# Kernel optimization log

Hardware: AMD Instinct MI355X
Metric: run time of the kernel (lower is better)

Reference implementation:

```python
import jax, jax.numpy as jnp
import numpy as np

EPS_OT = 0.05   # sinkhorn epsilon
ITERS = 3       # sinkhorn iterations
NH = 8          # attention heads


def _l2norm(x, axis):
    return x / jnp.maximum(jnp.linalg.norm(x, axis=axis, keepdims=True), 1e-12)


def _conv(x, w, pad):
    return jax.lax.conv_general_dilated(
        x, w, (1, 1), ((pad, pad), (pad, pad)),
        dimension_numbers=("NCHW", "OIHW", "NCHW"))


def _head(x, w1, b1, g, beta, w2, b2):
    # Conv3x3 -> BatchNorm (train-mode batch stats) -> ReLU -> Conv1x1
    h = _conv(x, w1, 1) + b1[None, :, None, None]
    mu = jnp.mean(h, (0, 2, 3), keepdims=True)
    var = jnp.var(h, (0, 2, 3), keepdims=True)
    h = jax.nn.relu((h - mu) / jnp.sqrt(var + 1e-5) * g[None, :, None, None]
                    + beta[None, :, None, None])
    return jnp.einsum("oc,bchw->bohw", w2, h) + b2[None, :, None, None]


def setup_inputs() -> dict:
    key = jax.random.key(0)
    ks = jax.random.split(key, 20)
    B, C, H, W, TD = 8, 256, 48, 48, 512
    s = 0.02
    f32 = jnp.float32
    d = {
        "img_feat": jax.random.normal(ks[0], (B, C, H, W), f32),
        "txt_feat": jax.random.normal(ks[1], (B, TD), f32),
        "density_map": jax.random.uniform(ks[2], (B, 1, H, W), f32),
        "tp_w": s * jax.random.normal(ks[3], (C, TD), f32), "tp_b": jnp.zeros((C,), f32),
        "wq": s * jax.random.normal(ks[4], (C, C), f32), "bq": jnp.zeros((C,), f32),
        "wk": s * jax.random.normal(ks[5], (C, C), f32), "bk": jnp.zeros((C,), f32),
        "wv": s * jax.random.normal(ks[6], (C, C), f32), "bv": jnp.zeros((C,), f32),
        "wo": s * jax.random.normal(ks[7], (C, C), f32), "bo": jnp.zeros((C,), f32),
        "ln_g": jnp.ones((C,), f32), "ln_b": jnp.zeros((C,), f32),
        "op_w": s * jax.random.normal(ks[8], (C, C), f32), "op_b": jnp.zeros((C,), f32),
        "h1_w": s * jax.random.normal(ks[9], (C // 2, C, 3, 3), f32), "h1_b": jnp.zeros((C // 2,), f32),
        "h_bn_g": jnp.ones((C // 2,), f32), "h_bn_b": jnp.zeros((C // 2,), f32),
        "h2_w": s * jax.random.normal(ks[10], (2, C // 2), f32), "h2_b": jnp.zeros((2,), f32),
        "v1_w": s * jax.random.normal(ks[11], (C // 2, C, 3, 3), f32), "v1_b": jnp.zeros((C // 2,), f32),
        "v_bn_g": jnp.ones((C // 2,), f32), "v_bn_b": jnp.zeros((C // 2,), f32),
        "v2_w": s * jax.random.normal(ks[12], (2, C // 2), f32), "v2_b": jnp.zeros((2,), f32),
        "temperature": 0.07 * jnp.ones((1,), f32),
        "spatial_weight": 0.1 * jnp.ones((1,), f32),
    }
    return d


def reference(img_feat, txt_feat, density_map, tp_w, tp_b, wq, bq, wk, bk,
              wv, bv, wo, bo, ln_g, ln_b, op_w, op_b, h1_w, h1_b, h_bn_g,
              h_bn_b, h2_w, h2_b, v1_w, v1_b, v_bn_g, v_bn_b, v2_w, v2_b,
              temperature, spatial_weight):
    B, C, H, W = img_feat.shape
    N = H * W
    hd = C // NH

    # ---- text projection (single text token) ----
    txt_emb = txt_feat @ tp_w.T + tp_b                      # [B,C]

    # ---- cross attention: query = pixels, key/value = 1 text token ----
    img_flat = img_feat.reshape(B, C, N).transpose(0, 2, 1)  # [B,N,C]
    q = (img_flat @ wq.T + bq).reshape(B, N, NH, hd)
    k = (txt_emb @ wk.T + bk).reshape(B, 1, NH, hd)
    v = (txt_emb @ wv.T + bv).reshape(B, 1, NH, hd)
    scores = jnp.einsum("bnhd,bkhd->bhnk", q, k) / jnp.sqrt(jnp.float32(hd))
    attn = jax.nn.softmax(scores, axis=-1)                  # ones (k len = 1)
    ctx = jnp.einsum("bhnk,bkhd->bnhd", attn, v).reshape(B, N, C)
    attn_out = ctx @ wo.T + bo

    # ---- residual + layernorm ----
    x = img_flat + attn_out
    mu = jnp.mean(x, -1, keepdims=True)
    var = jnp.var(x, -1, keepdims=True)
    source_feat = (x - mu) / jnp.sqrt(var + 1e-5) * ln_g + ln_b   # [B,N,C]
    mod_img_feat = source_feat.transpose(0, 2, 1).reshape(B, C, H, W)

    # ---- target distribution q from density map ----
    target = jax.nn.relu(density_map.reshape(B, N)) + 1e-6
    q_dist = target / jnp.sum(target, axis=1, keepdims=True)

    # ---- source distribution p from cosine similarity ----
    img_n = _l2norm(mod_img_feat, 1)                        # [B,C,H,W]
    txt_n = _l2norm(txt_emb, 1)                             # [B,C]
    cos = jnp.sum(img_n * txt_n[:, :, None, None], axis=1).reshape(B, N)
    temp = jnp.clip(temperature, 0.01, None)                # [1]
    logits = cos / temp
    mask = (cos > 0.0).astype(jnp.float32)
    shifted = logits - jnp.max(logits, axis=1, keepdims=True)
    p_un = jnp.exp(shifted) * mask + 1e-8
    p = p_un / jnp.sum(p_un, axis=1, keepdims=True)

    # ---- cost matrix: feature + spatial ----
    src_n = _l2norm(source_feat, 2)                         # [B,N,C]
    feature_cost = 1.0 - jnp.einsum("bnc,bmc->bnm", src_n, src_n)
    gy, gx = jnp.meshgrid(jnp.linspace(0.0, 1.0, H), jnp.linspace(0.0, 1.0, W),
                          indexing="ij")
    coords = jnp.stack([gy, gx], -1).reshape(N, 2)
    d2 = jnp.sum((coords[:, None, :] - coords[None, :, :]) ** 2, -1)
    spatial_cost = jnp.sqrt(jnp.maximum(d2, 0.0)) / 1.41421356  # [N,N]
    cost = feature_cost + spatial_weight * spatial_cost[None]   # [B,N,N]

    # ---- log-domain Sinkhorn ----
    log_p = jnp.log(p + 1e-12)
    log_q = jnp.log(q_dist + 1e-12)
    f = jnp.zeros_like(p)
    g = jnp.zeros_like(q_dist)
    for _ in range(ITERS):
        f = EPS_OT * (log_p - jax.scipy.special.logsumexp(
            (g[:, None, :] - cost) / EPS_OT, axis=2))
        g = EPS_OT * (log_q - jax.scipy.special.logsumexp(
            (f[:, :, None] - cost) / EPS_OT, axis=1))
    T = jnp.exp((f[:, :, None] + g[:, None, :] - cost) / EPS_OT)

    # ---- transport features: T^T @ source ----
    fused = jnp.einsum("bnm,bnc->bmc", T, source_feat)      # [B,N,C]
    fused_feat = fused.transpose(0, 2, 1).reshape(B, C, H, W)

    out_feat = img_feat + (jnp.einsum("oc,bchw->bohw", op_w, fused_feat)
                           + op_b[None, :, None, None])
    heatmap_logits = _head(out_feat, h1_w, h1_b, h_bn_g, h_bn_b, h2_w, h2_b)
    hv_logits = _head(out_feat, v1_w, v1_b, v_bn_g, v_bn_b, v2_w, v2_b)
    return out_feat, heatmap_logits, hv_logits
```

## Files before the change

kernel.cpp:

```cpp
#include <hip/hip_runtime.h>
#include <hip/hip_bf16.h>

#define NTOK 2304
#define CCH  256
#define BB   8

typedef __attribute__((ext_vector_type(4))) float f32x4;
typedef __attribute__((ext_vector_type(8))) short s16x8;
typedef __attribute__((ext_vector_type(8))) _Float16 h16x8;
typedef unsigned short u16;
typedef unsigned char u8;

__device__ __forceinline__ u16 f2bf(float x){
  union{float f; unsigned u;} v; v.f = x;
  unsigned r = v.u + 0x7fffu + ((v.u>>16)&1u);
  return (u16)(r>>16);
}
__device__ __forceinline__ float bf2f(u16 h){
  union{float f; unsigned u;} v; v.u = ((unsigned)h)<<16; return v.f;
}

#if __has_builtin(__builtin_amdgcn_cvt_f32_fp8) && __has_builtin(__builtin_amdgcn_cvt_pk_fp8_f32)
#define HWFP8 1
#else
#define HWFP8 0
#endif

__device__ __forceinline__ u8 enc8(float z){
  union{float f; unsigned u;} a; a.f = fabsf(z) * 0x1p-120f;
  unsigned u = a.u + 0x7FFFFu + ((a.u>>20)&1u);
  unsigned b = (u>>20)&0x7Fu;
  if (b > 0x7Eu) b = 0x7Eu;
  return (u8)(b | (z<0.f ? 0x80u : 0u));
}
__device__ __forceinline__ float dec8(unsigned b){
  union{unsigned u; float f;} w;
  w.u = ((b&0x80u)<<24) | ((b&0x7Fu)<<20);
  return w.f * 0x1p120f;
}

#if HWFP8
__device__ __forceinline__ float DEC8(unsigned w, int e){
  switch(e & 3){
    case 0:  return __builtin_amdgcn_cvt_f32_fp8((int)w, 0);
    case 1:  return __builtin_amdgcn_cvt_f32_fp8((int)w, 1);
    case 2:  return __builtin_amdgcn_cvt_f32_fp8((int)w, 2);
    default: return __builtin_amdgcn_cvt_f32_fp8((int)w, 3);
  }
}
__device__ __forceinline__ unsigned pack4(float z0,float z1,float z2,float z3){
  int v = __builtin_amdgcn_cvt_pk_fp8_f32(z0, z1, 0, false);
  v = __builtin_amdgcn_cvt_pk_fp8_f32(z2, z3, v, true);
  return (unsigned)v;
}
#else
__device__ __forceinline__ float DEC8(unsigned w, int e){
  return dec8((w>>(8*(e&3)))&0xFFu);
}
__device__ __forceinline__ unsigned pack4(float z0,float z1,float z2,float z3){
  return (unsigned)enc8(z0) | ((unsigned)enc8(z1)<<8) |
         ((unsigned)enc8(z2)<<16) | ((unsigned)enc8(z3)<<24);
}
#endif

__device__ __forceinline__ int swz512(int row, int b){ return row*512 + (b ^ ((row&7)<<4)); }
__device__ __forceinline__ int swz128(int row, int b){ return row*128 + (b ^ ((row&7)<<4)); }
__device__ __forceinline__ int swz64 (int row, int b){ return row*64  + (b ^ ((row&3)<<4)); }

__device__ __forceinline__ void gl_lds16(const void* g, void* l){
  __builtin_amdgcn_global_load_lds(
      (const __attribute__((address_space(1))) unsigned int*)g,
      (__attribute__((address_space(3))) unsigned int*)l, 16, 0, 0);
}

struct CanonArgs {
  const void* src[31];
  int n[31];
  int off[31];
};

__global__ void k_detect(const u16* probe, int* flag){
  if (threadIdx.x==0){
    int cnt=0;
    for (int i=0;i<16;++i){
      unsigned e = (probe[2*i]>>7)&0xFFu;
      if (e>=100u && e<=140u) ++cnt;
    }
    *flag = (cnt>=14)?1:0;
  }
}

__global__ __launch_bounds__(256) void k_canon(CanonArgs a, float* dst, const int* flag, int nt){
  int t = blockIdx.y;
  if (t>=nt) return;
  int n = a.n[t];
  const void* s = a.src[t];
  float* d = dst + a.off[t];
  bool isbf = (*flag)!=0;
  int n4 = n >> 2;
  for (int i = blockIdx.x*256+threadIdx.x; i < n4; i += gridDim.x*256){
    if (isbf){
      ushort4 v = ((const ushort4*)s)[i];
      float4 o; o.x=bf2f(v.x); o.y=bf2f(v.y); o.z=bf2f(v.z); o.w=bf2f(v.w);
      ((float4*)d)[i] = o;
    } else {
      ((float4*)d)[i] = ((const float4*)s)[i];
    }
  }
  int base = n4<<2;
  int rem = n - base;
  int i = blockIdx.x*256+threadIdx.x;
  if (i < rem)
    d[base+i] = isbf ? bf2f(((const u16*)s)[base+i]) : ((const float*)s)[base+i];
}

__global__ __launch_bounds__(256) void k_txt(const float* txt, const float* tpw, const float* tpb,
    const float* wv, const float* bv, const float* wo, const float* bo, float* TXTN, float* AVEC){
  int b=blockIdx.x, t=threadIdx.x;
  __shared__ float sT[512];
  __shared__ float sE[256];
  __shared__ float sV[256];
  __shared__ float red[4];
  sT[t]      = txt[b*512+t];
  sT[t+256]  = txt[b*512+256+t];
  __syncthreads();
  float acc = tpb[t];
  const float* wr = tpw + (size_t)t*512;
  for (int k=0;k<512;++k) acc = fmaf(sT[k], wr[k], acc);
  sE[t] = acc;
  float ss = acc*acc;
  for (int d=1; d<64; d<<=1) ss += __shfl_xor(ss, d);
  if ((t&63)==0) red[t>>6] = ss;
  __syncthreads();
  float nrm = sqrtf(red[0]+red[1]+red[2]+red[3]);
  TXTN[b*256+t] = acc / fmaxf(nrm, 1e-12f);
  float av = bv[t];
  const float* wvr = wv + (size_t)t*256;
  for (int k=0;k<256;++k) av = fmaf(sE[k], wvr[k], av);
  sV[t] = av;
  __syncthreads();
  float ao = bo[t];
  const float* wor = wo + (size_t)t*256;
  for (int k=0;k<256;++k) ao = fmaf(sV[k], wor[k], ao);
  AVEC[b*256+t] = ao;
}

__global__ __launch_bounds__(256) void k_lnfuse(const float* img, const float* AVEC, const float* lng,
    const float* lnb, const float* TXTN, u16* SF, u16* SN, float* COS){
  int b=blockIdx.y, n0=blockIdx.x*32, t=threadIdx.x;
  __shared__ float xt[32][256];
  float av = AVEC[b*256+t];
  const float* ip = img + ((size_t)b*256 + t)*NTOK + n0;
  #pragma unroll
  for (int j4=0;j4<8;++j4){
    float4 v = *(const float4*)(ip + j4*4);
    xt[j4*4+0][t]=v.x+av; xt[j4*4+1][t]=v.y+av; xt[j4*4+2][t]=v.z+av; xt[j4*4+3][t]=v.w+av;
  }
  int wv_=t>>6, l=t&63;
  float lg[4], lb[4], tn[4];
  #pragma unroll
  for (int k=0;k<4;++k){ lg[k]=lng[l+64*k]; lb[k]=lnb[l+64*k]; tn[k]=TXTN[b*256+l+64*k]; }
  __syncthreads();
  for (int rr=0; rr<8; ++rr){
    int j = wv_*8+rr; int n = n0+j;
    float x[4]; float s=0.f, ss=0.f;
    #pragma unroll
    for (int k=0;k<4;++k){ float v=xt[j][l+64*k]; x[k]=v; s+=v; ss=fmaf(v,v,ss); }
    for (int d=1; d<64; d<<=1){ s += __shfl_xor(s,d); ss += __shfl_xor(ss,d); }
    float mu = s*(1.f/256.f);
    float var = ss*(1.f/256.f) - mu*mu;
    float rstd = rsqrtf(fmaxf(var,0.f)+1e-5f);
    float y[4]; float sy=0.f;
    #pragma unroll
    for (int k=0;k<4;++k){ y[k] = fmaf((x[k]-mu)*rstd, lg[k], lb[k]); sy = fmaf(y[k],y[k],sy); }
    for (int d=1; d<64; d<<=1) sy += __shfl_xor(sy,d);
    float rn = 1.f/fmaxf(sqrtf(sy),1e-12f);
    float cp = 0.f;
    size_t base = ((size_t)b*NTOK + n)*CCH;
    #pragma unroll
    for (int k=0;k<4;++k){
      float sv = y[k]*rn;
      SF[base + l+64*k] = f2bf(y[k]);
      SN[base + l+64*k] = f2bf(sv);
      cp = fmaf(sv, tn[k], cp);
    }
    for (int d=1; d<64; d<<=1) cp += __shfl_xor(cp,d);
    if (l==0) COS[b*NTOK+n] = cp;
  }
}

__global__ __launch_bounds__(256) void k_pqred(const float* COS, const float* den, const float* tmpp, float* PQS){
  int b=blockIdx.x, t=threadIdx.x;
  __shared__ float red[256];
  float temp = fmaxf(tmpp[0], 0.01f);
  float mx = -1e30f;
  for (int n=t; n<NTOK; n+=256) mx = fmaxf(mx, COS[b*NTOK+n]);
  red[t]=mx; __syncthreads();
  for (int o=128;o>0;o>>=1){ if (t<o) red[t]=fmaxf(red[t],red[t+o]); __syncthreads(); }
  float maxc = red[0]; __syncthreads();
  float sp=0.f, st=0.f;
  for (int n=t; n<NTOK; n+=256){
    float cv = COS[b*NTOK+n];
    sp += __expf((cv-maxc)/temp)*((cv>0.f)?1.f:0.f)+1e-8f;
    float dv = den[b*NTOK+n];
    st += fmaxf(dv,0.f)+1e-6f;
  }
  red[t]=sp; __syncthreads();
  for (int o=128;o>0;o>>=1){ if (t<o) red[t]+=red[t+o]; __syncthreads(); }
  sp = red[0]; __syncthreads();
  red[t]=st; __syncthreads();
  for (int o=128;o>0;o>>=1){ if (t<o) red[t]+=red[t+o]; __syncthreads(); }
  if (t==0){ PQS[b*4]=maxc; PQS[b*4+1]=sp; PQS[b*4+2]=red[0]; }
}

__global__ __launch_bounds__(256) void k_pqelem(const float* COS, const float* den, const float* tmpp,
    const float* PQS, float* LOGP, float* LOGQ, float* GV, float* CY, float* CX){
  int idx = blockIdx.x*256+threadIdx.x;
  float temp = fmaxf(tmpp[0], 0.01f);
  if (idx < BB*NTOK){
    int b = idx / NTOK;
    float maxc = PQS[b*4], sp = PQS[b*4+1], st = PQS[b*4+2];
    float cv = COS[idx];
    float pu = __expf((cv-maxc)/temp)*((cv>0.f)?1.f:0.f)+1e-8f;
    LOGP[idx] = logf(pu/sp + 1e-12f);
    float dv = den[idx];
    LOGQ[idx] = logf((fmaxf(dv,0.f)+1e-6f)/st + 1e-12f);
    GV[idx] = 0.f;
  }
  if (idx < NTOK){
    int h = idx/48, w = idx - h*48;
    CY[idx] = (float)h*(1.f/47.f);
    CX[idx] = (float)w*(1.f/47.f);
  }
}

__global__ __launch_bounds__(256) void k_packw(const float* h1w, const float* v1w, u16* W1P){
  int idx = blockIdx.x*256+threadIdx.x;
  int head = idx / 294912;
  int rem = idx - head*294912;
  int oc = rem / 2304;
  int k = rem - oc*2304;
  int tap = k >> 8;
  int c = k & 255;
  const float* src = head ? v1w : h1w;
  W1P[idx] = f2bf(src[(oc*256 + c)*9 + tap]);
}

__global__ __launch_bounds__(256) void k_trans(const u16* SF, u16* SFT){
  int n0 = blockIdx.x*64, c0 = blockIdx.y*64, b = blockIdx.z;
  __shared__ u16 tl[64][68];
  int t = threadIdx.x;
  int nl = t>>3, c8 = (t&7)*8;
  #pragma unroll
  for (int p=0;p<2;++p){
    int n = nl + p*32;
    s16x8 v = *(const s16x8*)(SF + ((size_t)(b*NTOK + n0+n)*CCH + c0 + c8));
    #pragma unroll
    for (int e=0;e<8;++e) tl[c8+e][n] = (u16)v[e];
  }
  __syncthreads();
  int cl = t>>3, n8 = (t&7)*8;
  #pragma unroll
  for (int p=0;p<2;++p){
    int c = cl + p*32;
    union{ s16x8 v; u16 us[8]; } pk;
    #pragma unroll
    for (int e=0;e<8;++e){ int s = n8+e; pk.us[e] = tl[c][((s&3)<<4) | (s>>2)]; }
    *(s16x8*)(SFT + ((size_t)(b*CCH + c0+c)*NTOK + n0 + n8)) = pk.v;
  }
}

__global__ __launch_bounds__(256, 4) void k_cost(const u16* SN, const float* CY, const float* CX,
    const float* swp, u8* Z, float* PZ, int b_base){
  int zb = blockIdx.z, b = b_base + zb;
  int i0 = blockIdx.x*64, by = blockIdx.y, j0b = by*256;
  const u16* SNb = SN + (size_t)b*NTOK*CCH;
  u8* Zb = Z + (size_t)zb*NTOK*NTOK;
  __shared__ __align__(16) char Bs[64*512];
  int tid=threadIdx.x, w=tid>>6, l=tid&63, g4=l>>4, lc=l&15;
  float spw = swp[0]*(20.0f/1.41421356f);
  const u16* Arow = SNb + (size_t)(i0 + w*16 + lc)*CCH + g4*8;
  s16x8 af[8];
  #pragma unroll
  for (int ks=0; ks<8; ++ks) af[ks] = *(const s16x8*)(Arow + ks*32);
  int mrow = w*16 + g4*4;
  float cyi[4], cxi[4];
  #pragma unroll
  for (int r=0;r<4;++r){ int i = i0+mrow+r; cyi[r]=CY[i]; cxi[r]=CX[i]; }
  float Srow[4] = {0.f,0.f,0.f,0.f};
  for (int js=0; js<4; ++js){
    int j0 = j0b + js*64;
    __syncthreads();
    #pragma unroll
    for (int u=0; u<8; ++u){
      int row = u*8 + w*2 + (l>>5);
      int src = ((l&31)*16) ^ ((row&7)<<4);
      gl_lds16((const char*)(SNb + (size_t)(j0+row)*CCH) + src, Bs + u*4096 + w*1024);
    }
    __syncthreads();
    f32x4 acc[4];
    #pragma unroll
    for (int cf=0;cf<4;++cf) acc[cf] = (f32x4){0.f,0.f,0.f,0.f};
    #pragma unroll
    for (int ks=0; ks<8; ++ks){
      int kb = ks*64 + g4*16;
      #pragma unroll
      for (int cf=0; cf<4; ++cf){
        s16x8 bb = *(const s16x8*)(Bs + swz512(cf*16+lc, kb));
        acc[cf] = __builtin_amdgcn_mfma_f32_16x16x32_bf16(af[ks], bb, acc[cf], 0,0,0);
      }
    }
    float zf[4][4];
    #pragma unroll
    for (int cf=0; cf<4; ++cf){
      int j = j0 + cf*16 + lc;
      float cyj = CY[j], cxj = CX[j];
      #pragma unroll
      for (int r=0;r<4;++r){
        float dy = cyi[r]-cyj, dx = cxi[r]-cxj;
        zf[cf][r] = (acc[cf][r]-1.0f)*20.0f - spw*sqrtf(fmaf(dy,dy,dx*dx));
      }
    }
    size_t zrow = (size_t)(i0+mrow)*NTOK + j0 + lc*4;
    #pragma unroll
    for (int r=0;r<4;++r){
      unsigned pw = pack4(zf[0][r], zf[1][r], zf[2][r], zf[3][r]);
      Srow[r] += __expf(DEC8(pw,0)) + __expf(DEC8(pw,1))
               + __expf(DEC8(pw,2)) + __expf(DEC8(pw,3));
      *(unsigned*)(Zb + zrow + (size_t)r*NTOK) = pw;
    }
  }
  #pragma unroll
  for (int r=0;r<4;++r){
    float s = Srow[r];
    s += __shfl_xor(s,1); s += __shfl_xor(s,2); s += __shfl_xor(s,4); s += __shfl_xor(s,8);
    if (lc==0) PZ[(size_t)(zb*NTOK + i0 + mrow + r)*9 + by] = s;
  }
}

__global__ __launch_bounds__(256) void k_sinkred(const float* PZ, const float* LOGP, float* FV,
    int b_base, int zcnt){
  int idx = blockIdx.x*256 + threadIdx.x;
  if (idx >= zcnt*NTOK) return;
  int zb = idx / NTOK, row = idx - zb*NTOK, b = b_base + zb;
  const float* p = PZ + (size_t)idx*9;
  float s = 0.f;
  #pragma unroll
  for (int k=0;k<9;++k) s += p[k];
  FV[b*NTOK+row] = 0.05f*(LOGP[b*NTOK+row] - logf(s));
}

__global__ __launch_bounds__(256) void k_sinkZ(const u8* Z, const float* addv,
    const float* basev, float* outv, int b_base){
  int zb = blockIdx.y, b = b_base + zb, i0 = blockIdx.x*16;
  __shared__ float fs[NTOK];
  __shared__ float wm[4];
  int t = threadIdx.x;
  for (int j=t; j<NTOK; j+=256){
    int p = j & 63, tt = ((p&3)<<4) | (p>>2);
    fs[j] = addv[b*NTOK + (j & ~63) + tt]*20.f;
  }
  __syncthreads();
  float m = -1e30f;
  for (int j=t; j<NTOK; j+=256) m = fmaxf(m, fs[j]);
  #pragma unroll
  for (int d=1; d<64; d<<=1) m = fmaxf(m, __shfl_xor(m, d));
  if ((t&63)==0) wm[t>>6] = m;
  __syncthreads();
  float C = fmaxf(fmaxf(wm[0],wm[1]), fmaxf(wm[2],wm[3]));
  int rl = t>>4, q = t&15;
  int row = i0 + rl;
  const u8* zr = Z + ((size_t)zb*NTOK + row)*NTOK;
  float S = 0.f;
  for (int c0 = q*32; c0 < NTOK; c0 += 512){
    uint4 zA = *(const uint4*)(zr + c0);
    uint4 zB = *(const uint4*)(zr + c0 + 16);
    unsigned wd[8] = {zA.x,zA.y,zA.z,zA.w, zB.x,zB.y,zB.z,zB.w};
    float s32 = 0.f;
    #pragma unroll
    for (int k=0;k<8;++k)
      #pragma unroll
      for (int e=0;e<4;++e)
        s32 += __expf(fs[c0 + k*4 + e] + DEC8(wd[k], e) - C);
    S += s32;
  }
  #pragma unroll
  for (int d=1; d<16; d<<=1) S += __shfl_xor(S, d);
  if (q==0)
    outv[b*NTOK+row] = 0.05f*(basev[b*NTOK+row] - (C + logf(S)));
}

__global__ __launch_bounds__(256) void k_applyT(const u8* Z, const u16* SFT, const float* FVv,
    const float* GVv, u16* FU, int b_base){
  int zb = blockIdx.y, b = b_base + zb, m0 = blockIdx.x*64;
  __shared__ __align__(16) char WtL[64*128];
  __shared__ __align__(16) char BL[256*128];
  __shared__ float gs[64];
  __shared__ float sfv[NTOK];
  int tid=threadIdx.x, w=tid>>6, l=tid&63, g4=l>>4, lc=l&15;
  if (tid<64) gs[tid] = GVv[b*NTOK+m0+tid]*20.f;
  const float* Fv = FVv + b*NTOK;
  for (int j=tid; j<NTOK; j+=256){
    int p = j & 63, tt = ((p&3)<<4) | (p>>2);
    sfv[j] = Fv[(j & ~63) + tt]*20.f;
  }
  const u8* Zb = Z + ((size_t)zb*NTOK + m0)*NTOK;
  const u16* Bg = SFT + (size_t)b*CCH*NTOK + (size_t)tid*NTOK;
  f32x4 acc[4][4];
  #pragma unroll
  for (int mf=0;mf<4;++mf)
    #pragma unroll
    for (int cf=0;cf<4;++cf) acc[mf][cf] = (f32x4){0.f,0.f,0.f,0.f};
  int zm = tid>>2, zq = (tid&3)*16;
  for (int n0=0; n0<NTOK; n0+=64){
    uint4 zw = *(const uint4*)(Zb + (size_t)zm*NTOK + n0 + zq);
    s16x8 bv[8];
    #pragma unroll
    for (int u=0;u<8;++u) bv[u] = *(const s16x8*)(Bg + n0 + u*8);
    __syncthreads();
    {
      float g20 = gs[zm];
      unsigned wd[4] = {zw.x, zw.y, zw.z, zw.w};
      union{ s16x8 v; u16 us[8]; } w0, w1;
      #pragma unroll
      for (int col=0; col<16; ++col){
        float val = __expf(sfv[n0+zq+col] + g20 + DEC8(wd[col>>2], col&3));
        if (col < 8) w0.us[col] = f2bf(val); else w1.us[col-8] = f2bf(val);
      }
      *(s16x8*)(WtL + swz128(zm, zq*2)) = w0.v;
      *(s16x8*)(WtL + swz128(zm, zq*2+16)) = w1.v;
    }
    #pragma unroll
    for (int u=0;u<8;++u) *(s16x8*)(BL + swz128(tid, u*16)) = bv[u];
    __syncthreads();
    #pragma unroll
    for (int kk=0; kk<2; ++kk){
      s16x8 a[4];
      #pragma unroll
      for (int mf=0;mf<4;++mf) a[mf] = *(const s16x8*)(WtL + swz128(mf*16+lc, kk*64 + g4*16));
      #pragma unroll
      for (int cf=0; cf<4; ++cf){
        s16x8 bb = *(const s16x8*)(BL + swz128(w*64+cf*16+lc, kk*64 + g4*16));
        #pragma unroll
        for (int mf=0; mf<4; ++mf)
          acc[mf][cf] = __builtin_amdgcn_mfma_f32_16x16x32_bf16(a[mf], bb, acc[mf][cf], 0,0,0);
      }
    }
  }
  u16* FUb = FU + (size_t)b*NTOK*CCH;
  #pragma unroll
  for (int mf=0; mf<4; ++mf)
    #pragma unroll
    for (int cf=0; cf<4; ++cf)
      #pragma unroll
      for (int r=0;r<4;++r){
        int m = m0 + mf*16 + g4*4 + r;
        int c = w*64 + cf*16 + lc;
        FUb[(size_t)m*CCH + c] = f2bf(acc[mf][cf][r]);
      }
}

__global__ __launch_bounds__(256) void k_opgemm(const u16* FU, const float* opw, const float* opb,
    const float* img, float* dout, u16* OFN){
  int b=blockIdx.y, n0=blockIdx.x*64;
  __shared__ __align__(16) char Am[64*512];
  __shared__ __align__(16) char Bw[256*64];
  int tid=threadIdx.x, w=tid>>6, l=tid&63, g4=l>>4, lc=l&15;
  const u16* FUb = FU + (size_t)b*NTOK*CCH;
  for (int ch=tid; ch<64*32; ch+=256){
    int r=ch>>5, c8=(ch&31)*8;
    s16x8 v = *(const s16x8*)(FUb + (size_t)(n0+r)*CCH + c8);
    *(s16x8*)(Am + swz512(r, c8*2)) = v;
  }
  f32x4 acc[4][4];
  #pragma unroll
  for (int mf=0;mf<4;++mf)
    #pragma unroll
    for (int cf=0;cf<4;++cf) acc[mf][cf] = (f32x4){0.f,0.f,0.f,0.f};
  for (int ks=0; ks<8; ++ks){
    __syncthreads();
    {
      int o = tid;
      const float* wr = opw + (size_t)o*CCH + ks*32;
      #pragma unroll
      for (int u=0; u<4; ++u){
        float4 v0 = *(const float4*)(wr + u*8);
        float4 v1 = *(const float4*)(wr + u*8 + 4);
        union { s16x8 v; u16 us[8]; } pk;
        pk.us[0]=f2bf(v0.x); pk.us[1]=f2bf(v0.y); pk.us[2]=f2bf(v0.z); pk.us[3]=f2bf(v0.w);
        pk.us[4]=f2bf(v1.x); pk.us[5]=f2bf(v1.y); pk.us[6]=f2bf(v1.z); pk.us[7]=f2bf(v1.w);
        *(s16x8*)(Bw + swz64(o, u*16)) = pk.v;
      }
    }
    __syncthreads();
    #pragma unroll
    for (int mf=0; mf<4; ++mf){
      s16x8 a = *(const s16x8*)(Am + swz512(mf*16+lc, (ks*32+g4*8)*2));
      #pragma unroll
      for (int cf=0; cf<4; ++cf){
        int o = w*64+cf*16+lc;
        s16x8 bb = *(const s16x8*)(Bw + swz64(o, g4*16));
        acc[mf][cf] = __builtin_amdgcn_mfma_f32_16x16x32_bf16(a, bb, acc[mf][cf], 0,0,0);
      }
    }
  }
  #pragma unroll
  for (int mf=0; mf<4; ++mf){
    int nl = mf*16 + g4*4; int n = n0+nl;
    #pragma unroll
    for (int cf=0; cf<4; ++cf){
      int o = w*64+cf*16+lc;
      float ob = opb[o];
      const float* ip = img + ((size_t)b*CCH + o)*NTOK + n;
      float4 im = *(const float4*)ip;
      float o0 = acc[mf][cf][0]+ob+im.x;
      float o1 = acc[mf][cf][1]+ob+im.y;
      float o2 = acc[mf][cf][2]+ob+im.z;
      float o3 = acc[mf][cf][3]+ob+im.w;
      float4 st; st.x=o0; st.y=o1; st.z=o2; st.w=o3;
      *(float4*)(dout + ((size_t)b*CCH+o)*NTOK + n) = st;
      u16* ofp = OFN + ((size_t)b*NTOK + n)*CCH + o;
      ofp[0]=f2bf(o0); ofp[CCH]=f2bf(o1); ofp[2*CCH]=f2bf(o2); ofp[3*CCH]=f2bf(o3);
    }
  }
}

__global__ __launch_bounds__(256) void k_conv2(const u16* OFN, const u16* W1P,
    const float* h1b, const float* v1b, u16* H1, u16* H2){
  int b = blockIdx.y, n0 = blockIdx.x*64;
  __shared__ __align__(16) char As[64*128];
  __shared__ __align__(16) char Ws[256*128];
  int tid=threadIdx.x, w=tid>>6, l=tid&63, g4=l>>4, lc=l&15;
  int ar = tid>>2, aseg = (tid&3)*16;
  int arow = n0 + ar;
  int hr = arow/48, wc = arow - hr*48;
  const u16* Ob = OFN + (size_t)b*NTOK*CCH;
  const u16* Wg = W1P + (size_t)tid*2304;
  f32x4 acc[4][4];
  #pragma unroll
  for (int mf=0;mf<4;++mf)
    #pragma unroll
    for (int of=0;of<4;++of) acc[mf][of] = (f32x4){0.f,0.f,0.f,0.f};
  for (int kc=0; kc<36; ++kc){
    int tap = kc>>2, cq = (kc&3)*64;
    int kh = tap/3;
    int dh = kh-1, dw = (tap-kh*3)-1;
    bool val = ((unsigned)(hr+dh) < 48u) && ((unsigned)(wc+dw) < 48u);
    s16x8 a0 = {0,0,0,0,0,0,0,0}, a1 = {0,0,0,0,0,0,0,0};
    if (val){
      const u16* ap = Ob + (size_t)(arow + dh*48 + dw)*CCH + cq + aseg;
      a0 = *(const s16x8*)ap;
      a1 = *(const s16x8*)(ap+8);
    }
    const u16* wp = Wg + tap*256 + cq;
    s16x8 wv[8];
    #pragma unroll
    for (int u=0;u<8;++u) wv[u] = *(const s16x8*)(wp + u*8);
    __syncthreads();
    *(s16x8*)(As + swz128(ar, aseg*2))    = a0;
    *(s16x8*)(As + swz128(ar, aseg*2+16)) = a1;
    #pragma unroll
    for (int u=0;u<8;++u) *(s16x8*)(Ws + swz128(tid, u*16)) = wv[u];
    __syncthreads();
    #pragma unroll
    for (int ks=0; ks<2; ++ks){
      s16x8 af[4];
      #pragma unroll
      for (int mf=0;mf<4;++mf) af[mf] = *(const s16x8*)(As + swz128(mf*16+lc, ks*64 + g4*16));
      #pragma unroll
      for (int of=0; of<4; ++of){
        s16x8 bf = *(const s16x8*)(Ws + swz128(w*64+of*16+lc, ks*64 + g4*16));
        #pragma unroll
        for (int mf=0; mf<4; ++mf)
          acc[mf][of] = __builtin_amdgcn_mfma_f32_16x16x32_bf16(af[mf], bf, acc[mf][of], 0,0,0);
      }
    }
  }
  #pragma unroll
  for (int of=0; of<4; ++of){
    int o = w*64 + of*16 + lc;
    int head = o>>7, oc = o&127;
    float bias = (head? v1b : h1b)[oc];
    u16* Hh = head? H2 : H1;
    #pragma unroll
    for (int mf=0; mf<4; ++mf){
      #pragma unroll
      for (int r=0;r<4;++r){
        int n = n0 + mf*16 + g4*4 + r;
        Hh[((size_t)b*NTOK+n)*128 + oc] = f2bf(acc[mf][of][r] + bias);
      }
    }
  }
}

__global__ __launch_bounds__(128) void k_stats(const u16* H1, const u16* H2, float* PART){
  int head=blockIdx.y, blk=blockIdx.x, t=threadIdx.x;
  const u16* Hh = head? H2:H1;
  float s=0.f, ss=0.f;
  size_t r0 = (size_t)blk*288;
  for (int r=0;r<288;++r){
    float v = bf2f(Hh[(r0+r)*128 + t]);
    s += v; ss = fmaf(v,v,ss);
  }
  PART[((head*64+blk)*128+t)*2]   = s;
  PART[((head*64+blk)*128+t)*2+1] = ss;
}

__global__ __launch_bounds__(128) void k_statr(const float* PART, const float* hbg, const float* hbb,
    const float* vbg, const float* vbb, float* BNS){
  int head=blockIdx.x, t=threadIdx.x;
  float s=0.f, ss=0.f;
  for (int blk=0;blk<64;++blk){
    s  += PART[((head*64+blk)*128+t)*2];
    ss += PART[((head*64+blk)*128+t)*2+1];
  }
  float mean = s*(1.f/18432.f);
  float var = ss*(1.f/18432.f) - mean*mean;
  var = fmaxf(var, 0.f);
  const float* g  = head? vbg:hbg;
  const float* be = head? vbb:hbb;
  float sc = g[t]/sqrtf(var+1e-5f);
  BNS[(head*128+t)*2]   = sc;
  BNS[(head*128+t)*2+1] = be[t] - mean*sc;
}

__global__ __launch_bounds__(128) void k_fin(const u16* H1, const u16* H2, const float* BNS,
    const float* h2w, const float* h2b, const float* v2w, const float* v2b, float* dout){
  int head = blockIdx.z, b = blockIdx.y, n0 = blockIdx.x*128, t=threadIdx.x;
  const u16* Hh = head? H2:H1;
  const float* w2 = head? v2w:h2w;
  const float* b2 = head? v2b:h2b;
  __shared__ u16 tile[128][130];
  __shared__ float sc[128], bi[128], wa[128], wb[128];
  sc[t]=BNS[(head*128+t)*2]; bi[t]=BNS[(head*128+t)*2+1];
  wa[t]=w2[t]; wb[t]=w2[128+t];
  for (int r=0;r<128;++r) tile[r][t] = Hh[((size_t)b*NTOK+n0+r)*128 + t];
  __syncthreads();
  float a0=b2[0], a1=b2[1];
  for (int ch=0; ch<128; ++ch){
    float v = fmaf(bf2f(tile[t][ch]), sc[ch], bi[ch]);
    v = fmaxf(v, 0.f);
    a0 = fmaf(wa[ch], v, a0);
    a1 = fmaf(wb[ch], v, a1);
  }
  size_t base = (size_t)8*256*2304 + (size_t)head*36864 + (size_t)b*2*2304 + n0 + t;
  dout[base]        = a0;
  dout[base+2304]   = a1;
}

extern "C" void kernel_launch(void* const* d_in, const int* in_sizes, int n_in,
                              void* d_out, int out_size, void* d_ws, size_t ws_size,
                              hipStream_t stream){
  (void)out_size;
  long off[31]; long tot=0;
  int ni = n_in < 31 ? n_in : 31;
  for (int i=0;i<ni;++i){ off[i]=tot; tot += ((long)in_sizes[i]+63)&~63L; }
  char* ws = (char*)d_ws;
  size_t pos = 0;
  auto alloc = [&](size_t bytes)->char*{
    char* p = ws+pos; pos = (pos + bytes + 255) & ~(size_t)255; return p; };
  int*   FLAG = (int*)alloc(256);
  float* TXTN = (float*)alloc(8*256*4);
  float* AVEC = (float*)alloc(8*256*4);
  float* COS  = (float*)alloc(8*2304*4);
  float* LOGP = (float*)alloc(8*2304*4);
  float* LOGQ = (float*)alloc(8*2304*4);
  float* FV   = (float*)alloc(8*2304*4);
  float* GV   = (float*)alloc(8*2304*4);
  float* CY   = (float*)alloc(2304*4);
  float* CX   = (float*)alloc(2304*4);
  float* PQS  = (float*)alloc(8*4*4);
  float* PART = (float*)alloc(2*64*128*2*4);
  float* BNS  = (float*)alloc(2*128*2*4);
  float* PZ   = (float*)alloc((size_t)8*2304*9*4);
  u16* W1P = (u16*)alloc((size_t)2*128*9*256*2);
  u16* SF  = (u16*)alloc((size_t)8*2304*256*2);
  u16* SN  = (u16*)alloc((size_t)8*2304*256*2);
  u16* SFT = (u16*)alloc((size_t)8*2304*256*2);
  u16* FU  = (u16*)alloc((size_t)8*2304*256*2);
  u16* OFN = (u16*)alloc((size_t)8*2304*256*2);
  u16* H1  = (u16*)alloc((size_t)8*2304*128*2);
  u16* H2  = (u16*)alloc((size_t)8*2304*128*2);
  float* canon = (float*)alloc((size_t)tot*4);
  size_t zslice = (size_t)NTOK*NTOK;
  int zsl = (pos + 8*zslice + 256 <= ws_size) ? 8 : 1;
  u8* Z = (u8*)alloc((size_t)zsl*zslice);

  k_detect<<<1,64,0,stream>>>((const u16*)d_in[1], FLAG);
  CanonArgs ca;
  for (int i=0;i<ni;++i){ ca.src[i]=d_in[i]; ca.n[i]=in_sizes[i]; ca.off[i]=(int)off[i]; }
  k_canon<<<dim3(512,(unsigned)ni),256,0,stream>>>(ca, canon, FLAG, ni);

  const float* c_img = canon+off[0];
  const float* c_txt = canon+off[1];
  const float* c_den = canon+off[2];
  const float* c_tpw = canon+off[3];
  const float* c_tpb = canon+off[4];
  const float* c_wv  = canon+off[9];
  const float* c_bv  = canon+off[10];
  const float* c_wo  = canon+off[11];
  const float* c_bo  = canon+off[12];
  const float* c_lng = canon+off[13];
  const float* c_lnb = canon+off[14];
  const float* c_opw = canon+off[15];
  const float* c_opb = canon+off[16];
  const float* c_h1w = canon+off[17];
  const float* c_h1b = canon+off[18];
  const float* c_hbg = canon+off[19];
  const float* c_hbb = canon+off[20];
  const float* c_h2w = canon+off[21];
  const float* c_h2b = canon+off[22];
  const float* c_v1w = canon+off[23];
  const float* c_v1b = canon+off[24];
  const float* c_vbg = canon+off[25];
  const float* c_vbb = canon+off[26];
  const float* c_v2w = canon+off[27];
  const float* c_v2b = canon+off[28];
  const float* c_tmp = canon+off[29];
  const float* c_sw  = canon+off[30];

  k_txt<<<8,256,0,stream>>>(c_txt, c_tpw, c_tpb, c_wv, c_bv, c_wo, c_bo, TXTN, AVEC);
  k_lnfuse<<<dim3(72,8),256,0,stream>>>(c_img, AVEC, c_lng, c_lnb, TXTN, SF, SN, COS);
  k_pqred<<<8,256,0,stream>>>(COS, c_den, c_tmp, PQS);
  k_pqelem<<<80,256,0,stream>>>(COS, c_den, c_tmp, PQS, LOGP, LOGQ, GV, CY, CX);
  k_packw<<<2304,256,0,stream>>>(c_h1w, c_v1w, W1P);
  k_trans<<<dim3(36,4,8),256,0,stream>>>(SF, SFT);

  if (zsl == 8){
    k_cost<<<dim3(36,9,8),256,0,stream>>>(SN, CY, CX, c_sw, Z, PZ, 0);
    k_sinkred<<<72,256,0,stream>>>(PZ, LOGP, FV, 0, 8);
    for (int it=0; it<3; ++it){
      if (it>0) k_sinkZ<<<dim3(144,8),256,0,stream>>>(Z, GV, LOGP, FV, 0);
      k_sinkZ<<<dim3(144,8),256,0,stream>>>(Z, FV, LOGQ, GV, 0);
    }
    k_applyT<<<dim3(36,8),256,0,stream>>>(Z, SFT, FV, GV, FU, 0);
  } else {
    for (int bi=0; bi<8; ++bi){
      k_cost<<<dim3(36,9,1),256,0,stream>>>(SN, CY, CX, c_sw, Z, PZ, bi);
      k_sinkred<<<9,256,0,stream>>>(PZ, LOGP, FV, bi, 1);
      for (int it=0; it<3; ++it){
        if (it>0) k_sinkZ<<<dim3(144,1),256,0,stream>>>(Z, GV, LOGP, FV, bi);
        k_sinkZ<<<dim3(144,1),256,0,stream>>>(Z, FV, LOGQ, GV, bi);
      }
      k_applyT<<<dim3(36,1),256,0,stream>>>(Z, SFT, FV, GV, FU, bi);
    }
  }

  k_opgemm<<<dim3(36,8),256,0,stream>>>(FU, c_opw, c_opb, c_img, (float*)d_out, OFN);
  k_conv2<<<dim3(36,8),256,0,stream>>>(OFN, W1P, c_h1b, c_v1b, H1, H2);
  k_stats<<<dim3(64,2),128,0,stream>>>(H1, H2, PART);
  k_statr<<<2,128,0,stream>>>(PART, c_hbg, c_hbb, c_vbg, c_vbb, BNS);
  k_fin<<<dim3(18,8,2),128,0,stream>>>(H1, H2, BNS, c_h2w, c_h2b, c_v2w, c_v2b, (float*)d_out);
}
```

Baseline: 423.9 us.

## Split applyT over K with atomic accumulation, async LDS loads, and larger sinkZ tiles

k_applyT now splits the 2304-long reduction across two blocks (grid 36x2x8). Partial results are accumulated with fp32 atomicAdd into a zeroed fp32 buffer, which k_opgemm converts to bf16 when it loads. The B operand is staged with direct global-to-LDS loads (gl_lds16), and the next Z tile is prefetched into registers. k_sinkZ processes 32 rows per block with 8 lanes per row instead of 16, so it launches fewer blocks. The intent is more parallelism in applyT (288 to 576 blocks) and less register staging, at the cost of an extra zeroing pass, twice the FU buffer traffic, and atomic contention.

```diff
diff --git a/kernel.cpp b/kernel.cpp
--- a/kernel.cpp
+++ b/kernel.cpp
@@ -4,6 +4,7 @@
 #define NTOK 2304
 #define CCH  256
 #define BB   8
+#define NSPL 2
 
 typedef __attribute__((ext_vector_type(4))) float f32x4;
 typedef __attribute__((ext_vector_type(8))) short s16x8;
@@ -112,6 +113,11 @@
   int i = blockIdx.x*256+threadIdx.x;
   if (i < rem)
     d[base+i] = isbf ? bf2f(((const u16*)s)[base+i]) : ((const float*)s)[base+i];
+}
+
+__global__ __launch_bounds__(256) void k_zero(float* p, int n4){
+  int i = blockIdx.x*256+threadIdx.x;
+  if (i < n4) ((float4*)p)[i] = (float4){0.f,0.f,0.f,0.f};
 }
 
 __global__ __launch_bounds__(256) void k_txt(const float* txt, const float* tpw, const float* tpb,
@@ -352,7 +358,7 @@
 
 __global__ __launch_bounds__(256) void k_sinkZ(const u8* Z, const float* addv,
     const float* basev, float* outv, int b_base){
-  int zb = blockIdx.y, b = b_base + zb, i0 = blockIdx.x*16;
+  int zb = blockIdx.y, b = b_base + zb, i0 = blockIdx.x*32;
   __shared__ float fs[NTOK];
   __shared__ float wm[4];
   int t = threadIdx.x;
@@ -368,11 +374,11 @@
   if ((t&63)==0) wm[t>>6] = m;
   __syncthreads();
   float C = fmaxf(fmaxf(wm[0],wm[1]), fmaxf(wm[2],wm[3]));
-  int rl = t>>4, q = t&15;
+  int rl = t>>3, q = t&7;
   int row = i0 + rl;
   const u8* zr = Z + ((size_t)zb*NTOK + row)*NTOK;
   float S = 0.f;
-  for (int c0 = q*32; c0 < NTOK; c0 += 512){
+  for (int c0 = q*32; c0 < NTOK; c0 += 256){
     uint4 zA = *(const uint4*)(zr + c0);
     uint4 zB = *(const uint4*)(zr + c0 + 16);
     unsigned wd[8] = {zA.x,zA.y,zA.z,zA.w, zB.x,zB.y,zB.z,zB.w};
@@ -385,53 +391,62 @@
     S += s32;
   }
   #pragma unroll
-  for (int d=1; d<16; d<<=1) S += __shfl_xor(S, d);
+  for (int d=1; d<8; d<<=1) S += __shfl_xor(S, d);
   if (q==0)
     outv[b*NTOK+row] = 0.05f*(basev[b*NTOK+row] - (C + logf(S)));
 }
 
-__global__ __launch_bounds__(256) void k_applyT(const u8* Z, const u16* SFT, const float* FVv,
-    const float* GVv, u16* FU, int b_base){
-  int zb = blockIdx.y, b = b_base + zb, m0 = blockIdx.x*64;
+__global__ __launch_bounds__(256, 3) void k_applyT(const u8* Z, const u16* SFT, const float* FVv,
+    const float* GVv, float* FUF, int b_base){
+  int zb = blockIdx.z, b = b_base + zb, m0 = blockIdx.x*64;
+  int sp = blockIdx.y;
+  int nbeg = sp*(NTOK/NSPL), nend = nbeg + (NTOK/NSPL);
   __shared__ __align__(16) char WtL[64*128];
   __shared__ __align__(16) char BL[256*128];
   __shared__ float gs[64];
-  __shared__ float sfv[NTOK];
+  __shared__ float sfv[NTOK/NSPL];
   int tid=threadIdx.x, w=tid>>6, l=tid&63, g4=l>>4, lc=l&15;
   if (tid<64) gs[tid] = GVv[b*NTOK+m0+tid]*20.f;
   const float* Fv = FVv + b*NTOK;
-  for (int j=tid; j<NTOK; j+=256){
-    int p = j & 63, tt = ((p&3)<<4) | (p>>2);
-    sfv[j] = Fv[(j & ~63) + tt]*20.f;
+  for (int j=tid; j<NTOK/NSPL; j+=256){
+    int jj = nbeg + j;
+    int p = jj & 63, tt = ((p&3)<<4) | (p>>2);
+    sfv[j] = Fv[(jj & ~63) + tt]*20.f;
   }
   const u8* Zb = Z + ((size_t)zb*NTOK + m0)*NTOK;
-  const u16* Bg = SFT + (size_t)b*CCH*NTOK + (size_t)tid*NTOK;
+  const u16* SFTb = SFT + (size_t)b*CCH*NTOK;
   f32x4 acc[4][4];
   #pragma unroll
   for (int mf=0;mf<4;++mf)
     #pragma unroll
     for (int cf=0;cf<4;++cf) acc[mf][cf] = (f32x4){0.f,0.f,0.f,0.f};
   int zm = tid>>2, zq = (tid&3)*16;
-  for (int n0=0; n0<NTOK; n0+=64){
-    uint4 zw = *(const uint4*)(Zb + (size_t)zm*NTOK + n0 + zq);
-    s16x8 bv[8];
-    #pragma unroll
-    for (int u=0;u<8;++u) bv[u] = *(const s16x8*)(Bg + n0 + u*8);
+  int lrow = l>>3;
+  int lsrc = ((l&7)*16) ^ (lrow<<4);
+  uint4 zwc = *(const uint4*)(Zb + (size_t)zm*NTOK + nbeg + zq);
+  for (int n0=nbeg; n0<nend; n0+=64){
     __syncthreads();
+    int nn = (n0+64 < nend) ? n0+64 : nbeg;
+    uint4 zwn = *(const uint4*)(Zb + (size_t)zm*NTOK + nn + zq);
+    #pragma unroll
+    for (int u=0; u<8; ++u){
+      int row = w*64 + u*8 + lrow;
+      gl_lds16((const char*)(SFTb + (size_t)row*NTOK) + n0*2 + lsrc,
+               BL + (w*64 + u*8)*128);
+    }
     {
       float g20 = gs[zm];
-      unsigned wd[4] = {zw.x, zw.y, zw.z, zw.w};
+      unsigned wd[4] = {zwc.x, zwc.y, zwc.z, zwc.w};
       union{ s16x8 v; u16 us[8]; } w0, w1;
+      int sbase = n0 - nbeg + zq;
       #pragma unroll
       for (int col=0; col<16; ++col){
-        float val = __expf(sfv[n0+zq+col] + g20 + DEC8(wd[col>>2], col&3));
+        float val = __expf(sfv[sbase+col] + g20 + DEC8(wd[col>>2], col&3));
         if (col < 8) w0.us[col] = f2bf(val); else w1.us[col-8] = f2bf(val);
       }
       *(s16x8*)(WtL + swz128(zm, zq*2)) = w0.v;
       *(s16x8*)(WtL + swz128(zm, zq*2+16)) = w1.v;
     }
-    #pragma unroll
-    for (int u=0;u<8;++u) *(s16x8*)(BL + swz128(tid, u*16)) = bv[u];
     __syncthreads();
     #pragma unroll
     for (int kk=0; kk<2; ++kk){
@@ -446,8 +461,9 @@
           acc[mf][cf] = __builtin_amdgcn_mfma_f32_16x16x32_bf16(a[mf], bb, acc[mf][cf], 0,0,0);
       }
     }
-  }
-  u16* FUb = FU + (size_t)b*NTOK*CCH;
+    zwc = zwn;
+  }
+  float* FUb = FUF + (size_t)b*NTOK*CCH;
   #pragma unroll
   for (int mf=0; mf<4; ++mf)
     #pragma unroll
@@ -456,21 +472,26 @@
       for (int r=0;r<4;++r){
         int m = m0 + mf*16 + g4*4 + r;
         int c = w*64 + cf*16 + lc;
-        FUb[(size_t)m*CCH + c] = f2bf(acc[mf][cf][r]);
-      }
-}
-
-__global__ __launch_bounds__(256) void k_opgemm(const u16* FU, const float* opw, const float* opb,
+        atomicAdd(&FUb[(size_t)m*CCH + c], acc[mf][cf][r]);
+      }
+}
+
+__global__ __launch_bounds__(256) void k_opgemm(const float* FUF, const float* opw, const float* opb,
     const float* img, float* dout, u16* OFN){
   int b=blockIdx.y, n0=blockIdx.x*64;
   __shared__ __align__(16) char Am[64*512];
   __shared__ __align__(16) char Bw[256*64];
   int tid=threadIdx.x, w=tid>>6, l=tid&63, g4=l>>4, lc=l&15;
-  const u16* FUb = FU + (size_t)b*NTOK*CCH;
+  const float* FUb = FUF + (size_t)b*NTOK*CCH;
   for (int ch=tid; ch<64*32; ch+=256){
     int r=ch>>5, c8=(ch&31)*8;
-    s16x8 v = *(const s16x8*)(FUb + (size_t)(n0+r)*CCH + c8);
-    *(s16x8*)(Am + swz512(r, c8*2)) = v;
+    const float* fp = FUb + (size_t)(n0+r)*CCH + c8;
+    float4 v0 = *(const float4*)fp;
+    float4 v1 = *(const float4*)(fp+4);
+    union { s16x8 v; u16 us[8]; } pk;
+    pk.us[0]=f2bf(v0.x); pk.us[1]=f2bf(v0.y); pk.us[2]=f2bf(v0.z); pk.us[3]=f2bf(v0.w);
+    pk.us[4]=f2bf(v1.x); pk.us[5]=f2bf(v1.y); pk.us[6]=f2bf(v1.z); pk.us[7]=f2bf(v1.w);
+    *(s16x8*)(Am + swz512(r, c8*2)) = pk.v;
   }
   f32x4 acc[4][4];
   #pragma unroll
@@ -677,7 +698,7 @@
   u16* SF  = (u16*)alloc((size_t)8*2304*256*2);
   u16* SN  = (u16*)alloc((size_t)8*2304*256*2);
   u16* SFT = (u16*)alloc((size_t)8*2304*256*2);
-  u16* FU  = (u16*)alloc((size_t)8*2304*256*2);
+  float* FUF = (float*)alloc((size_t)8*2304*256*4);
   u16* OFN = (u16*)alloc((size_t)8*2304*256*2);
   u16* H1  = (u16*)alloc((size_t)8*2304*128*2);
   u16* H2  = (u16*)alloc((size_t)8*2304*128*2);
@@ -690,6 +711,7 @@
   CanonArgs ca;
   for (int i=0;i<ni;++i){ ca.src[i]=d_in[i]; ca.n[i]=in_sizes[i]; ca.off[i]=(int)off[i]; }
   k_canon<<<dim3(512,(unsigned)ni),256,0,stream>>>(ca, canon, FLAG, ni);
+  k_zero<<<4608,256,0,stream>>>(FUF, 8*2304*256/4);
 
   const float* c_img = canon+off[0];
   const float* c_txt = canon+off[1];
@@ -730,23 +752,23 @@
     k_cost<<<dim3(36,9,8),256,0,stream>>>(SN, CY, CX, c_sw, Z, PZ, 0);
     k_sinkred<<<72,256,0,stream>>>(PZ, LOGP, FV, 0, 8);
     for (int it=0; it<3; ++it){
-      if (it>0) k_sinkZ<<<dim3(144,8),256,0,stream>>>(Z, GV, LOGP, FV, 0);
-      k_sinkZ<<<dim3(144,8),256,0,stream>>>(Z, FV, LOGQ, GV, 0);
-    }
-    k_applyT<<<dim3(36,8),256,0,stream>>>(Z, SFT, FV, GV, FU, 0);
+      if (it>0) k_sinkZ<<<dim3(72,8),256,0,stream>>>(Z, GV, LOGP, FV, 0);
+      k_sinkZ<<<dim3(72,8),256,0,stream>>>(Z, FV, LOGQ, GV, 0);
+    }
+    k_applyT<<<dim3(36,NSPL,8),256,0,stream>>>(Z, SFT, FV, GV, FUF, 0);
   } else {
     for (int bi=0; bi<8; ++bi){
       k_cost<<<dim3(36,9,1),256,0,stream>>>(SN, CY, CX, c_sw, Z, PZ, bi);
       k_sinkred<<<9,256,0,stream>>>(PZ, LOGP, FV, bi, 1);
       for (int it=0; it<3; ++it){
-        if (it>0) k_sinkZ<<<dim3(144,1),256,0,stream>>>(Z, GV, LOGP, FV, bi);
-        k_sinkZ<<<dim3(144,1),256,0,stream>>>(Z, FV, LOGQ, GV, bi);
-      }
-      k_applyT<<<dim3(36,1),256,0,stream>>>(Z, SFT, FV, GV, FU, bi);
-    }
-  }
-
-  k_opgemm<<<dim3(36,8),256,0,stream>>>(FU, c_opw, c_opb, c_img, (float*)d_out, OFN);
+        if (it>0) k_sinkZ<<<dim3(72,1),256,0,stream>>>(Z, GV, LOGP, FV, bi);
+        k_sinkZ<<<dim3(72,1),256,0,stream>>>(Z, FV, LOGQ, GV, bi);
+      }
+      k_applyT<<<dim3(36,NSPL,1),256,0,stream>>>(Z, SFT, FV, GV, FUF, bi);
+    }
+  }
+
+  k_opgemm<<<dim3(36,8),256,0,stream>>>(FUF, c_opw, c_opb, c_img, (float*)d_out, OFN);
   k_conv2<<<dim3(36,8),256,0,stream>>>(OFN, W1P, c_h1b, c_v1b, H1, H2);
   k_stats<<<dim3(64,2),128,0,stream>>>(H1, H2, PART);
   k_statr<<<2,128,0,stream>>>(PART, c_hbg, c_hbb, c_vbg, c_vbb, BNS);
```

Result: faster. 412.0 us (-2.8%).
